# Kernel optimization log

Measured on AMD Instinct MI355X. Metric: run time of the kernel, lower is better.

Reference implementation:

```python
import jax, jax.numpy as jnp
import numpy as np

GRID_MIN, GRID_MAX, NUM_GRIDS = -2.0, 2.0, 8
DENOM = (GRID_MAX - GRID_MIN) / (NUM_GRIDS - 1)
DIM, NUM_HEADS = 768, 12
B, N = 8, 1024


def _layer_norm(x, w, b, eps=1e-5):
    mu = jnp.mean(x, axis=-1, keepdims=True)
    var = jnp.mean((x - mu) ** 2, axis=-1, keepdims=True)
    return (x - mu) * jax.lax.rsqrt(var + eps) * w + b


def _fastkan(x, ln_w, ln_b, spline_w, base_w, base_b):
    # x: [..., C]; spline_w: [C*G, O]; base_w: [C, O]
    grid = jnp.linspace(GRID_MIN, GRID_MAX, NUM_GRIDS, dtype=x.dtype)
    h = _layer_norm(x, ln_w, ln_b)
    # RBF basis expansion: [..., C, G]
    basis = jnp.exp(-(((h[..., None] - grid) / DENOM) ** 2))
    basis = basis.reshape(*basis.shape[:-2], -1)  # [..., C*G]
    ret = basis @ spline_w
    ret = ret + jax.nn.silu(x) @ base_w + base_b
    return ret


def setup_inputs() -> dict:
    key = jax.random.key(0)
    ks = jax.random.split(key, 6)
    C = DIM
    return {
        "x": jax.random.normal(ks[0], (B, N, C), jnp.float32),
        "qkv_ln_w": jnp.ones((C,), jnp.float32),
        "qkv_ln_b": jnp.zeros((C,), jnp.float32),
        "qkv_spline_w": jax.random.normal(ks[1], (C * NUM_GRIDS, 3 * C), jnp.float32) * 0.1,
        "qkv_base_w": jax.random.normal(ks[2], (C, 3 * C), jnp.float32) * (1.0 / np.sqrt(C)),
        "qkv_base_b": jnp.zeros((3 * C,), jnp.float32),
        "proj_ln_w": jnp.ones((C,), jnp.float32),
        "proj_ln_b": jnp.zeros((C,), jnp.float32),
        "proj_spline_w": jax.random.normal(ks[3], (C * NUM_GRIDS, C), jnp.float32) * 0.1,
        "proj_base_w": jax.random.normal(ks[4], (C, C), jnp.float32) * (1.0 / np.sqrt(C)),
        "proj_base_b": jnp.zeros((C,), jnp.float32),
    }


def reference(x, qkv_ln_w, qkv_ln_b, qkv_spline_w, qkv_base_w, qkv_base_b,
              proj_ln_w, proj_ln_b, proj_spline_w, proj_base_w, proj_base_b):
    b, n, c = x.shape
    h = NUM_HEADS
    d = c // h
    scale = d ** -0.5
    qkv = _fastkan(x, qkv_ln_w, qkv_ln_b, qkv_spline_w, qkv_base_w, qkv_base_b)
    qkv = qkv.reshape(b, n, 3, h, d).transpose(2, 0, 3, 1, 4)  # [3,B,H,N,D]
    q, k, v = qkv[0], qkv[1], qkv[2]
    attn = jnp.einsum("bhnd,bhmd->bhnm", q, k) * scale
    attn = jax.nn.softmax(attn, axis=-1)
    out = jnp.einsum("bhnm,bhmd->bhnd", attn, v)
    out = out.transpose(0, 2, 1, 3).reshape(b, n, c)
    out = _fastkan(out, proj_ln_w, proj_ln_b, proj_spline_w, proj_base_w, proj_base_b)
    return out
```

## Files before the change

kernel.cpp:

```cpp
#include <hip/hip_runtime.h>
#include <cstdint>
#include <cstddef>

typedef _Float16 h8 __attribute__((ext_vector_type(8)));
typedef float f4 __attribute__((ext_vector_type(4)));
typedef float f16f __attribute__((ext_vector_type(16)));

#define DEV static __device__ __forceinline__

DEV void gld16(const void* g, void* l) {
  __builtin_amdgcn_global_load_lds(
      (const __attribute__((address_space(1))) void*)g,
      (__attribute__((address_space(3))) void*)l, 16, 0, 0);
}

__global__ __launch_bounds__(256)
void kan_prep(const float* __restrict__ X, const float* __restrict__ lnw,
              const float* __restrict__ lnb, _Float16* __restrict__ Acat) {
  const int row = blockIdx.x;
  const int tid = threadIdx.x;
  const float* xr = X + (size_t)row * 768;
  float xv[3];
  xv[0] = xr[tid]; xv[1] = xr[tid + 256]; xv[2] = xr[tid + 512];
  float s = xv[0] + xv[1] + xv[2];
  float q = xv[0] * xv[0] + xv[1] * xv[1] + xv[2] * xv[2];
#pragma unroll
  for (int off = 32; off; off >>= 1) {
    s += __shfl_xor(s, off);
    q += __shfl_xor(q, off);
  }
  __shared__ float rs_[4], rq_[4];
  const int wave = tid >> 6;
  if ((tid & 63) == 0) { rs_[wave] = s; rq_[wave] = q; }
  __syncthreads();
  s = rs_[0] + rs_[1] + rs_[2] + rs_[3];
  q = rq_[0] + rq_[1] + rq_[2] + rq_[3];
  const float mu = s * (1.0f / 768.0f);
  const float var = q * (1.0f / 768.0f) - mu * mu;
  const float rsig = rsqrtf(var + 1e-5f);
  _Float16* out = Acat + (size_t)row * 6912;
#pragma unroll
  for (int i = 0; i < 3; ++i) {
    const int c = tid + i * 256;
    const float x = xv[i];
    const float h = (x - mu) * rsig * lnw[c] + lnb[c];
    union { h8 v; _Float16 u[8]; } bs;
#pragma unroll
    for (int g = 0; g < 8; ++g) {
      const float gv = -2.0f + (4.0f / 7.0f) * (float)g;
      const float t = (h - gv) * 1.75f;
      bs.u[g] = (_Float16)__expf(-t * t);
    }
    *(h8*)(out + c * 8) = bs.v;
    out[6144 + c] = (_Float16)(x / (1.0f + __expf(-x)));
  }
}

__global__ __launch_bounds__(256)
void wt_cast(const float* __restrict__ W, _Float16* __restrict__ Bp,
             int N, int koff, int nkt) {
  __shared__ float t[32][33];
  const int k0 = blockIdx.x * 32, n0 = blockIdx.y * 32;
  const int tx = threadIdx.x & 31, ty = threadIdx.x >> 5;
#pragma unroll
  for (int i = 0; i < 4; ++i)
    t[ty + i * 8][tx] = W[(size_t)(k0 + ty + i * 8) * N + n0 + tx];
  __syncthreads();
  const int f = threadIdx.x;
  if (f < 128) {
    const int nn = f & 31, cc = f >> 5;
    union { h8 v; _Float16 u[8]; } bs;
#pragma unroll
    for (int j = 0; j < 8; ++j) bs.u[j] = (_Float16)t[cc * 8 + j][nn];
    const int kg = koff + k0 + cc * 8;
    const int nt = (n0 + nn) >> 5;
    const size_t addr = ((size_t)nt * nkt + (kg >> 6)) * 2048 +
                        (size_t)((((kg >> 4) & 3) * 64 + nn + 32 * ((kg >> 3) & 1))) * 8;
    *(h8*)(Bp + addr) = bs.v;
  }
}

__global__ __launch_bounds__(256)
void v_transpose(const _Float16* __restrict__ qkv, _Float16* __restrict__ Vt) {
  const int bh = blockIdx.z, hh = bh % 12, b = bh / 12;
  const int kvb = blockIdx.x * 32, db = blockIdx.y * 32;
  __shared__ _Float16 t[32][33];
  const int tx = threadIdx.x & 31, ty = threadIdx.x >> 5;
#pragma unroll
  for (int i = 0; i < 4; ++i) {
    const int kv = kvb + ty + i * 8;
    t[ty + i * 8][tx] = qkv[(size_t)(b * 1024 + kv) * 2304 + 1536 + hh * 64 + db + tx];
  }
  __syncthreads();
#pragma unroll
  for (int i = 0; i < 4; ++i) {
    const int d = db + ty + i * 8;
    Vt[(size_t)(bh * 64 + d) * 1024 + kvb + tx] = t[tx][ty + i * 8];
  }
}

template <bool F16OUT>
__global__ __launch_bounds__(256, 3)
void gemm_bt(const _Float16* __restrict__ A, const _Float16* __restrict__ Bp,
             const float* __restrict__ bias, void* __restrict__ Cout,
             int N, int ldK, int kLen, size_t sliceStride) {
  __shared__ __align__(16) _Float16 As[128 * 64];
  const int tid = threadIdx.x;
  const int lane = tid & 63, wave = tid >> 6;
  const int bm = blockIdx.y * 128, bn = blockIdx.x * 128;
  const int slice = blockIdx.z;
  const int kOff = slice * kLen;
  const int rsub = lane >> 3;
  const int l7 = lane & 7;
  const int l31 = lane & 31, half = lane >> 5;
  const int wm = (wave >> 1) * 64, wn = (wave & 1) * 64;
  const _Float16* ap[4];
  _Float16* al[4];
#pragma unroll
  for (int i = 0; i < 4; ++i) {
    const int ch = wave * 4 + i;
    const int ksw = (l7 ^ rsub ^ ((ch & 3) << 1)) * 8;
    ap[i] = A + (size_t)(bm + ch * 8 + rsub) * ldK + kOff + ksw;
    al[i] = As + ch * 512;
  }
  const size_t nktTot = (size_t)(ldK >> 6);
  const int kt0 = kOff >> 6;
  const _Float16* bpp[2];
#pragma unroll
  for (int ni = 0; ni < 2; ++ni)
    bpp[ni] = Bp + ((size_t)((bn >> 5) + (wn >> 5) + ni) * nktTot + kt0) * 2048 + lane * 8;

  f16f acc[2][2] = {};
  const int swz = l7 ^ ((rsub & 3) << 1);
  const int nkt = kLen >> 6;
  for (int kt = 0; kt < nkt; ++kt) {
    h8 breg[2][4];
#pragma unroll
    for (int ni = 0; ni < 2; ++ni)
#pragma unroll
      for (int ks = 0; ks < 4; ++ks)
        breg[ni][ks] = *(const h8*)(bpp[ni] + ks * 512);
#pragma unroll
    for (int i = 0; i < 4; ++i) {
      gld16(ap[i], al[i]);
      ap[i] += 64;
    }
#pragma unroll
    for (int ni = 0; ni < 2; ++ni) bpp[ni] += 2048;
    __syncthreads();
    const h8* A8 = (const h8*)As;
#pragma unroll
    for (int ks = 0; ks < 4; ++ks) {
      const int o = (ks * 2 + half) ^ swz;
      h8 af[2];
#pragma unroll
      for (int mi = 0; mi < 2; ++mi) af[mi] = A8[(wm + mi * 32 + l31) * 8 + o];
#pragma unroll
      for (int mi = 0; mi < 2; ++mi)
#pragma unroll
        for (int ni = 0; ni < 2; ++ni)
          acc[mi][ni] = __builtin_amdgcn_mfma_f32_32x32x16_f16(af[mi], breg[ni][ks], acc[mi][ni], 0, 0, 0);
    }
    __syncthreads();
  }
#pragma unroll
  for (int ni = 0; ni < 2; ++ni) {
    const int col = bn + wn + ni * 32 + l31;
    const float bv = F16OUT ? bias[col] : 0.0f;
#pragma unroll
    for (int mi = 0; mi < 2; ++mi) {
      const int rb = bm + wm + mi * 32 + 4 * half;
#pragma unroll
      for (int reg = 0; reg < 16; ++reg) {
        const int r = rb + (reg & 3) + 8 * (reg >> 2);
        const float v = acc[mi][ni][reg] + bv;
        if (F16OUT)
          ((_Float16*)Cout)[(size_t)r * N + col] = (_Float16)v;
        else
          ((float*)Cout + slice * sliceStride)[(size_t)r * N + col] = v;
      }
    }
  }
}

__global__ __launch_bounds__(256)
void ksum2(const float* __restrict__ P, const float* __restrict__ bias,
           float* __restrict__ out) {
  const size_t off = ((size_t)blockIdx.x * 256 + threadIdx.x) * 4;
  const int col = (int)(off % 768);
  f4 a = *(const f4*)(P + off);
  f4 b = *(const f4*)(P + (size_t)8192 * 768 + off);
  f4 c = *(const f4*)(bias + col);
  *(f4*)(out + off) = a + b + c;
}

__global__ __launch_bounds__(256)
void attn(const _Float16* __restrict__ qkv, const _Float16* __restrict__ Vt,
          float* __restrict__ ctx) {
  __shared__ __align__(16) _Float16 Qs[128 * 64];
  __shared__ __align__(16) _Float16 Ks[64 * 64];
  __shared__ __align__(16) _Float16 Vs[64 * 64];
  __shared__ __align__(16) _Float16 Ps[4 * 32 * 72];
  const int tid = threadIdx.x;
  const int lane = tid & 63, wave = tid >> 6;
  const int bh = blockIdx.y, hh = bh % 12, b = bh / 12;
  const int qt = blockIdx.x;
  const int rsub = lane >> 3;
  const int ksw = ((lane & 7) ^ rsub) * 8;
#pragma unroll
  for (int i = 0; i < 4; ++i) {
    const int ch = wave * 4 + i;
    const int row = ch * 8 + rsub;
    gld16(qkv + (size_t)(b * 1024 + qt * 128 + row) * 2304 + hh * 64 + ksw, Qs + ch * 512);
  }
  const int l16 = lane & 15, quad = lane >> 4, r7 = l16 & 7;
  f4 acc_o[2][4] = {};
  float m_old[2][4], l_sum[2][4];
#pragma unroll
  for (int mi = 0; mi < 2; ++mi)
#pragma unroll
    for (int j = 0; j < 4; ++j) { m_old[mi][j] = -1e30f; l_sum[mi][j] = 0.0f; }

  _Float16* Pw = Ps + wave * (32 * 72);

  for (int kv0 = 0; kv0 < 1024; kv0 += 64) {
#pragma unroll
    for (int i = 0; i < 2; ++i) {
      const int ch = wave * 2 + i;
      const int row = ch * 8 + rsub;
      gld16(qkv + (size_t)(b * 1024 + kv0 + row) * 2304 + 768 + hh * 64 + ksw, Ks + ch * 512);
      gld16(Vt + (size_t)(bh * 64 + row) * 1024 + kv0 + ksw, Vs + ch * 512);
    }
    __syncthreads();
    const h8* Q8 = (const h8*)Qs;
    const h8* K8 = (const h8*)Ks;
    const h8* V8 = (const h8*)Vs;
    f4 s[2][4] = {};
#pragma unroll
    for (int ks = 0; ks < 2; ++ks) {
      const int kq = (ks * 4 + quad) ^ r7;
      h8 qf[2], kf[4];
#pragma unroll
      for (int mi = 0; mi < 2; ++mi) qf[mi] = Q8[(wave * 32 + mi * 16 + l16) * 8 + kq];
#pragma unroll
      for (int ni = 0; ni < 4; ++ni) kf[ni] = K8[(ni * 16 + l16) * 8 + kq];
#pragma unroll
      for (int mi = 0; mi < 2; ++mi)
#pragma unroll
        for (int ni = 0; ni < 4; ++ni)
          s[mi][ni] = __builtin_amdgcn_mfma_f32_16x16x32_f16(qf[mi], kf[ni], s[mi][ni], 0, 0, 0);
    }
#pragma unroll
    for (int mi = 0; mi < 2; ++mi)
#pragma unroll
      for (int ni = 0; ni < 4; ++ni) s[mi][ni] *= 0.125f;
#pragma unroll
    for (int mi = 0; mi < 2; ++mi) {
#pragma unroll
      for (int j = 0; j < 4; ++j) {
        float vm = fmaxf(fmaxf(s[mi][0][j], s[mi][1][j]), fmaxf(s[mi][2][j], s[mi][3][j]));
#pragma unroll
        for (int off = 1; off < 16; off <<= 1) vm = fmaxf(vm, __shfl_xor(vm, off));
        const float mn = fmaxf(m_old[mi][j], vm);
        const float alpha = __expf(m_old[mi][j] - mn);
        float rs = 0.0f;
#pragma unroll
        for (int ni = 0; ni < 4; ++ni) {
          const float p = __expf(s[mi][ni][j] - mn);
          s[mi][ni][j] = p;
          rs += p;
        }
#pragma unroll
        for (int off = 1; off < 16; off <<= 1) rs += __shfl_xor(rs, off);
        l_sum[mi][j] = l_sum[mi][j] * alpha + rs;
        m_old[mi][j] = mn;
#pragma unroll
        for (int ni = 0; ni < 4; ++ni) acc_o[mi][ni][j] *= alpha;
      }
    }
#pragma unroll
    for (int mi = 0; mi < 2; ++mi)
#pragma unroll
      for (int ni = 0; ni < 4; ++ni)
#pragma unroll
        for (int j = 0; j < 4; ++j)
          Pw[(mi * 16 + quad * 4 + j) * 72 + ni * 16 + l16] = (_Float16)s[mi][ni][j];
#pragma unroll
    for (int ks = 0; ks < 2; ++ks) {
      const int kq = ks * 4 + quad;
      h8 pf[2], vf[4];
#pragma unroll
      for (int mi = 0; mi < 2; ++mi) pf[mi] = *(const h8*)(Pw + (mi * 16 + l16) * 72 + kq * 8);
#pragma unroll
      for (int ni = 0; ni < 4; ++ni) vf[ni] = V8[(ni * 16 + l16) * 8 + (kq ^ r7)];
#pragma unroll
      for (int mi = 0; mi < 2; ++mi)
#pragma unroll
        for (int ni = 0; ni < 4; ++ni)
          acc_o[mi][ni] = __builtin_amdgcn_mfma_f32_16x16x32_f16(pf[mi], vf[ni], acc_o[mi][ni], 0, 0, 0);
    }
    __syncthreads();
  }
#pragma unroll
  for (int mi = 0; mi < 2; ++mi) {
#pragma unroll
    for (int j = 0; j < 4; ++j) {
      const float inv = 1.0f / l_sum[mi][j];
      const int tok = b * 1024 + qt * 128 + wave * 32 + mi * 16 + quad * 4 + j;
      float* cr = ctx + (size_t)tok * 768 + hh * 64;
#pragma unroll
      for (int ni = 0; ni < 4; ++ni) cr[ni * 16 + l16] = acc_o[mi][ni][j] * inv;
    }
  }
}

extern "C" void kernel_launch(void* const* d_in, const int* in_sizes, int n_in,
                              void* d_out, int out_size, void* d_ws, size_t ws_size,
                              hipStream_t stream) {
  (void)in_sizes; (void)n_in; (void)out_size; (void)ws_size;
  const float* x    = (const float*)d_in[0];
  const float* qlnw = (const float*)d_in[1];
  const float* qlnb = (const float*)d_in[2];
  const float* qsw  = (const float*)d_in[3];
  const float* qbw  = (const float*)d_in[4];
  const float* qbb  = (const float*)d_in[5];
  const float* plnw = (const float*)d_in[6];
  const float* plnb = (const float*)d_in[7];
  const float* psw  = (const float*)d_in[8];
  const float* pbw  = (const float*)d_in[9];
  const float* pbb  = (const float*)d_in[10];
  float* out = (float*)d_out;

  _Float16* WtQ  = (_Float16*)d_ws;
  _Float16* WtP  = WtQ + (size_t)2304 * 6912;
  _Float16* Acat = WtP + (size_t)768 * 6912;
  _Float16* QKV  = Acat + (size_t)8192 * 6912;
  _Float16* Vt   = QKV + (size_t)8192 * 2304;
  float* CTX = (float*)(Vt + (size_t)96 * 64 * 1024);
  float* Pp = (float*)QKV;

  dim3 blk(256);
  wt_cast<<<dim3(192, 72), blk, 0, stream>>>(qsw, WtQ, 2304, 0, 108);
  wt_cast<<<dim3(24, 72),  blk, 0, stream>>>(qbw, WtQ, 2304, 6144, 108);
  wt_cast<<<dim3(192, 24), blk, 0, stream>>>(psw, WtP, 768, 0, 108);
  wt_cast<<<dim3(24, 24),  blk, 0, stream>>>(pbw, WtP, 768, 6144, 108);
  kan_prep<<<8192, blk, 0, stream>>>(x, qlnw, qlnb, Acat);
  gemm_bt<true><<<dim3(2304 / 128, 8192 / 128, 1), blk, 0, stream>>>(
      Acat, WtQ, qbb, QKV, 2304, 6912, 6912, 0);
  v_transpose<<<dim3(32, 2, 96), blk, 0, stream>>>(QKV, Vt);
  attn<<<dim3(8, 96), blk, 0, stream>>>(QKV, Vt, CTX);
  kan_prep<<<8192, blk, 0, stream>>>(CTX, plnw, plnb, Acat);
  gemm_bt<false><<<dim3(768 / 128, 8192 / 128, 2), blk, 0, stream>>>(
      Acat, WtP, nullptr, Pp, 768, 6912, 3456, (size_t)8192 * 768);
  ksum2<<<8192 * 768 / 4 / 256, blk, 0, stream>>>(Pp, pbb, out);
}
```

Measured before the change: 762.6 us.

## Double-buffer A tiles and B registers in gemm_bt with XCD-aware block remap

Software-pipelines the GEMM main loop: A tiles go to alternating LDS buffers and B fragments to alternating register sets, so the next K tile is fetched while MFMAs run on the current one. This hides global load latency behind compute. It also remaps block indices so that each XCD handles a contiguous band of M rows, aiming for better L2 reuse. In exchange, LDS use doubles and launch bounds drop to 2 blocks per CU. The remap assumes gridDim.y is divisible by 8, and the loop handles an odd tile count only through its guards.

```diff
diff --git a/kernel.cpp b/kernel.cpp
--- a/kernel.cpp
+++ b/kernel.cpp
@@ -99,15 +99,51 @@
   }
 }
 
+#define LOAD_B(dst)                                       \
+  {                                                       \
+    _Pragma("unroll") for (int ni = 0; ni < 2; ++ni) {    \
+      _Pragma("unroll") for (int ks = 0; ks < 4; ++ks)    \
+        dst[ni][ks] = *(const h8*)(bpp[ni] + ks * 512);   \
+      bpp[ni] += 2048;                                    \
+    }                                                     \
+  }
+#define LOAD_A(buf)                                       \
+  {                                                       \
+    _Pragma("unroll") for (int i = 0; i < 4; ++i) {       \
+      gld16(ap[i], (buf) + alOff[i]);                     \
+      ap[i] += 64;                                        \
+    }                                                     \
+  }
+#define MFMA_STEP(buf, br)                                \
+  {                                                       \
+    const h8* A8 = (const h8*)(buf);                      \
+    _Pragma("unroll") for (int ks = 0; ks < 4; ++ks) {    \
+      const int o = (ks * 2 + half) ^ swz;                \
+      h8 af0 = A8[(wm + l31) * 8 + o];                    \
+      h8 af1 = A8[(wm + 32 + l31) * 8 + o];               \
+      acc[0][0] = __builtin_amdgcn_mfma_f32_32x32x16_f16(af0, br[0][ks], acc[0][0], 0, 0, 0); \
+      acc[0][1] = __builtin_amdgcn_mfma_f32_32x32x16_f16(af0, br[1][ks], acc[0][1], 0, 0, 0); \
+      acc[1][0] = __builtin_amdgcn_mfma_f32_32x32x16_f16(af1, br[0][ks], acc[1][0], 0, 0, 0); \
+      acc[1][1] = __builtin_amdgcn_mfma_f32_32x32x16_f16(af1, br[1][ks], acc[1][1], 0, 0, 0); \
+    }                                                     \
+  }
+
 template <bool F16OUT>
-__global__ __launch_bounds__(256, 3)
+__global__ __launch_bounds__(256, 2)
 void gemm_bt(const _Float16* __restrict__ A, const _Float16* __restrict__ Bp,
              const float* __restrict__ bias, void* __restrict__ Cout,
              int N, int ldK, int kLen, size_t sliceStride) {
-  __shared__ __align__(16) _Float16 As[128 * 64];
+  __shared__ __align__(16) _Float16 As[2 * 128 * 64];
+  _Float16* As0 = As;
+  _Float16* As1 = As + 128 * 64;
   const int tid = threadIdx.x;
   const int lane = tid & 63, wave = tid >> 6;
-  const int bm = blockIdx.y * 128, bn = blockIdx.x * 128;
+  const int gx = gridDim.x;
+  const int lin = blockIdx.y * gx + blockIdx.x;
+  const int xcd = lin & 7, pos = lin >> 3;
+  const int bandH = gridDim.y >> 3;
+  const int bm = (xcd * bandH + pos / gx) * 128;
+  const int bn = (pos % gx) * 128;
   const int slice = blockIdx.z;
   const int kOff = slice * kLen;
   const int rsub = lane >> 3;
@@ -115,13 +151,13 @@
   const int l31 = lane & 31, half = lane >> 5;
   const int wm = (wave >> 1) * 64, wn = (wave & 1) * 64;
   const _Float16* ap[4];
-  _Float16* al[4];
+  int alOff[4];
 #pragma unroll
   for (int i = 0; i < 4; ++i) {
     const int ch = wave * 4 + i;
     const int ksw = (l7 ^ rsub ^ ((ch & 3) << 1)) * 8;
     ap[i] = A + (size_t)(bm + ch * 8 + rsub) * ldK + kOff + ksw;
-    al[i] = As + ch * 512;
+    alOff[i] = ch * 512;
   }
   const size_t nktTot = (size_t)(ldK >> 6);
   const int kt0 = kOff >> 6;
@@ -133,35 +169,16 @@
   f16f acc[2][2] = {};
   const int swz = l7 ^ ((rsub & 3) << 1);
   const int nkt = kLen >> 6;
-  for (int kt = 0; kt < nkt; ++kt) {
-    h8 breg[2][4];
-#pragma unroll
-    for (int ni = 0; ni < 2; ++ni)
-#pragma unroll
-      for (int ks = 0; ks < 4; ++ks)
-        breg[ni][ks] = *(const h8*)(bpp[ni] + ks * 512);
-#pragma unroll
-    for (int i = 0; i < 4; ++i) {
-      gld16(ap[i], al[i]);
-      ap[i] += 64;
-    }
-#pragma unroll
-    for (int ni = 0; ni < 2; ++ni) bpp[ni] += 2048;
+  h8 bregA[2][4], bregB[2][4];
+  LOAD_B(bregA);
+  LOAD_A(As0);
+  for (int kt = 0; kt < nkt; kt += 2) {
     __syncthreads();
-    const h8* A8 = (const h8*)As;
-#pragma unroll
-    for (int ks = 0; ks < 4; ++ks) {
-      const int o = (ks * 2 + half) ^ swz;
-      h8 af[2];
-#pragma unroll
-      for (int mi = 0; mi < 2; ++mi) af[mi] = A8[(wm + mi * 32 + l31) * 8 + o];
-#pragma unroll
-      for (int mi = 0; mi < 2; ++mi)
-#pragma unroll
-        for (int ni = 0; ni < 2; ++ni)
-          acc[mi][ni] = __builtin_amdgcn_mfma_f32_32x32x16_f16(af[mi], breg[ni][ks], acc[mi][ni], 0, 0, 0);
-    }
+    if (kt + 1 < nkt) { LOAD_B(bregB); LOAD_A(As1); }
+    MFMA_STEP(As0, bregA);
     __syncthreads();
+    if (kt + 2 < nkt) { LOAD_B(bregA); LOAD_A(As0); }
+    MFMA_STEP(As1, bregB);
   }
 #pragma unroll
   for (int ni = 0; ni < 2; ++ni) {
```

Result: faster. 698.8 us (-8.4%).

## Fuse RBF basis expansion into GEMM A-operand generation, store only normalized h

Applied to the files above, without the earlier changes.

Stops materializing the full 8x-expanded fp16 basis matrix. The prep kernel now writes normalized h transposed per channel, plus SiLU values in an MFMA fragment layout. The GEMM recomputes the eight RBF exponentials in registers per fragment, loads B directly into double-buffered registers, and drops the LDS A tile and barriers. This cuts global traffic for the large A matrix. The cost is much more exp work inside the GEMM (every N-tile block recomputes it), scattered 2-byte Ht loads, lower occupancy (launch bounds 2), and a grid swapped so blocks iterate M fastest.

```diff
diff --git a/kernel.cpp b/kernel.cpp
--- a/kernel.cpp
+++ b/kernel.cpp
@@ -14,45 +14,63 @@
       (__attribute__((address_space(3))) void*)l, 16, 0, 0);
 }
 
-__global__ __launch_bounds__(256)
-void kan_prep(const float* __restrict__ X, const float* __restrict__ lnw,
-              const float* __restrict__ lnb, _Float16* __restrict__ Acat) {
-  const int row = blockIdx.x;
-  const int tid = threadIdx.x;
-  const float* xr = X + (size_t)row * 768;
-  float xv[3];
-  xv[0] = xr[tid]; xv[1] = xr[tid + 256]; xv[2] = xr[tid + 512];
-  float s = xv[0] + xv[1] + xv[2];
-  float q = xv[0] * xv[0] + xv[1] * xv[1] + xv[2] * xv[2];
-#pragma unroll
-  for (int off = 32; off; off >>= 1) {
-    s += __shfl_xor(s, off);
-    q += __shfl_xor(q, off);
-  }
-  __shared__ float rs_[4], rq_[4];
-  const int wave = tid >> 6;
-  if ((tid & 63) == 0) { rs_[wave] = s; rq_[wave] = q; }
+DEV h8 rbf8(float h) {
+  const float a = fmaf(h, 1.75f, 3.5f);
+  union { h8 v; _Float16 u[8]; } o;
+#pragma unroll
+  for (int g = 0; g < 8; ++g) {
+    const float d = a - (float)g;
+    o.u[g] = (_Float16)__expf(-d * d);
+  }
+  return o.v;
+}
+
+__global__ __launch_bounds__(256)
+void kan_prep2(const float* __restrict__ X, const float* __restrict__ lnw,
+               const float* __restrict__ lnb, _Float16* __restrict__ Ht,
+               _Float16* __restrict__ Sf) {
+  const int mb = blockIdx.x;
+  const int R = mb * 32;
+  const int t = threadIdx.x;
+  __shared__ float mu_[32], rs_[32];
+  {
+    const int r = t >> 3, p = t & 7;
+    const float* xr = X + (size_t)(R + r) * 768;
+    float s = 0.f, q = 0.f;
+    for (int i = 0; i < 96; ++i) {
+      const float v = xr[p + 8 * i];
+      s += v; q += v * v;
+    }
+    s += __shfl_xor(s, 1); q += __shfl_xor(q, 1);
+    s += __shfl_xor(s, 2); q += __shfl_xor(q, 2);
+    s += __shfl_xor(s, 4); q += __shfl_xor(q, 4);
+    if (p == 0) {
+      const float mu = s * (1.f / 768.f);
+      mu_[r] = mu;
+      rs_[r] = rsqrtf(q * (1.f / 768.f) - mu * mu + 1e-5f);
+    }
+  }
   __syncthreads();
-  s = rs_[0] + rs_[1] + rs_[2] + rs_[3];
-  q = rq_[0] + rq_[1] + rq_[2] + rq_[3];
-  const float mu = s * (1.0f / 768.0f);
-  const float var = q * (1.0f / 768.0f) - mu * mu;
-  const float rsig = rsqrtf(var + 1e-5f);
-  _Float16* out = Acat + (size_t)row * 6912;
-#pragma unroll
-  for (int i = 0; i < 3; ++i) {
-    const int c = tid + i * 256;
-    const float x = xv[i];
-    const float h = (x - mu) * rsig * lnw[c] + lnb[c];
-    union { h8 v; _Float16 u[8]; } bs;
+  const int r = t & 31, cb = t >> 5;
+  const float mu = mu_[r], rsg = rs_[r];
+  for (int i = 0; i < 96; ++i) {
+    const int c = cb + 8 * i;
+    const float x = X[(size_t)(R + r) * 768 + c];
+    const float h = (x - mu) * rsg * lnw[c] + lnb[c];
+    Ht[(size_t)c * 8192 + R + r] = (_Float16)h;
+  }
+  for (int j = 0; j < 12; ++j) {
+    const int cc = cb + 8 * j;
+    const float* xp = X + (size_t)(R + r) * 768 + cc * 8;
+    union { h8 v; _Float16 u[8]; } sv;
 #pragma unroll
     for (int g = 0; g < 8; ++g) {
-      const float gv = -2.0f + (4.0f / 7.0f) * (float)g;
-      const float t = (h - gv) * 1.75f;
-      bs.u[g] = (_Float16)__expf(-t * t);
-    }
-    *(h8*)(out + c * 8) = bs.v;
-    out[6144 + c] = (_Float16)(x / (1.0f + __expf(-x)));
+      const float x = xp[g];
+      sv.u[g] = (_Float16)(x / (1.f + __expf(-x)));
+    }
+    const size_t addr = ((size_t)mb * 12 + (cc >> 3)) * 2048 +
+                        (size_t)(((cc >> 1) & 3) * 64 + r + 32 * (cc & 1)) * 8;
+    *(h8*)(Sf + addr) = sv.v;
   }
 }
 
@@ -99,69 +117,77 @@
   }
 }
 
+#define LOADB(dst, ktv)                                                   \
+  { _Pragma("unroll") for (int ni = 0; ni < 2; ++ni)                      \
+      _Pragma("unroll") for (int ks = 0; ks < 4; ++ks)                    \
+        dst[ni][ks] = *(const h8*)(bpp[ni] + (size_t)(ktv) * 2048 + ks * 512); }
+
+#define LOADH(dst, kgv)                                                   \
+  { _Pragma("unroll") for (int mi = 0; mi < 2; ++mi)                      \
+      _Pragma("unroll") for (int ks = 0; ks < 4; ++ks)                    \
+        dst[mi][ks] = Ht[(size_t)((kgv) * 8 + ks * 2 + half) * 8192 + am0 + mi * 32]; }
+
+#define STEP(bc, hc, kgv)                                                 \
+  {                                                                       \
+    if ((kgv) < 96) {                                                     \
+      _Pragma("unroll") for (int ks = 0; ks < 4; ++ks) {                  \
+        h8 a0 = rbf8((float)hc[0][ks]);                                   \
+        h8 a1 = rbf8((float)hc[1][ks]);                                   \
+        acc[0][0] = __builtin_amdgcn_mfma_f32_32x32x16_f16(a0, bc[0][ks], acc[0][0], 0, 0, 0); \
+        acc[0][1] = __builtin_amdgcn_mfma_f32_32x32x16_f16(a0, bc[1][ks], acc[0][1], 0, 0, 0); \
+        acc[1][0] = __builtin_amdgcn_mfma_f32_32x32x16_f16(a1, bc[0][ks], acc[1][0], 0, 0, 0); \
+        acc[1][1] = __builtin_amdgcn_mfma_f32_32x32x16_f16(a1, bc[1][ks], acc[1][1], 0, 0, 0); \
+      }                                                                   \
+    } else {                                                              \
+      const size_t tb = (size_t)((kgv) - 96) * 2048;                      \
+      _Pragma("unroll") for (int ks = 0; ks < 4; ++ks) {                  \
+        h8 a0 = *(const h8*)(Sf + sfB0 + tb + ks * 512);                  \
+        h8 a1 = *(const h8*)(Sf + sfB1 + tb + ks * 512);                  \
+        acc[0][0] = __builtin_amdgcn_mfma_f32_32x32x16_f16(a0, bc[0][ks], acc[0][0], 0, 0, 0); \
+        acc[0][1] = __builtin_amdgcn_mfma_f32_32x32x16_f16(a0, bc[1][ks], acc[0][1], 0, 0, 0); \
+        acc[1][0] = __builtin_amdgcn_mfma_f32_32x32x16_f16(a1, bc[0][ks], acc[1][0], 0, 0, 0); \
+        acc[1][1] = __builtin_amdgcn_mfma_f32_32x32x16_f16(a1, bc[1][ks], acc[1][1], 0, 0, 0); \
+      }                                                                   \
+    }                                                                     \
+  }
+
 template <bool F16OUT>
-__global__ __launch_bounds__(256, 3)
-void gemm_bt(const _Float16* __restrict__ A, const _Float16* __restrict__ Bp,
-             const float* __restrict__ bias, void* __restrict__ Cout,
-             int N, int ldK, int kLen, size_t sliceStride) {
-  __shared__ __align__(16) _Float16 As[128 * 64];
+__global__ __launch_bounds__(256, 2)
+void gemm_fused(const _Float16* __restrict__ Ht, const _Float16* __restrict__ Sf,
+                const _Float16* __restrict__ Bp, const float* __restrict__ bias,
+                void* __restrict__ Cout, int N, int ktPerSlice, int nktTot,
+                size_t sliceStride) {
   const int tid = threadIdx.x;
   const int lane = tid & 63, wave = tid >> 6;
-  const int bm = blockIdx.y * 128, bn = blockIdx.x * 128;
+  const int bm = blockIdx.x * 128, bn = blockIdx.y * 128;
   const int slice = blockIdx.z;
-  const int kOff = slice * kLen;
-  const int rsub = lane >> 3;
-  const int l7 = lane & 7;
+  const int kt0 = slice * ktPerSlice;
   const int l31 = lane & 31, half = lane >> 5;
   const int wm = (wave >> 1) * 64, wn = (wave & 1) * 64;
-  const _Float16* ap[4];
-  _Float16* al[4];
-#pragma unroll
-  for (int i = 0; i < 4; ++i) {
-    const int ch = wave * 4 + i;
-    const int ksw = (l7 ^ rsub ^ ((ch & 3) << 1)) * 8;
-    ap[i] = A + (size_t)(bm + ch * 8 + rsub) * ldK + kOff + ksw;
-    al[i] = As + ch * 512;
-  }
-  const size_t nktTot = (size_t)(ldK >> 6);
-  const int kt0 = kOff >> 6;
+  const int am0 = bm + wm + l31;
+  const size_t sfB0 = ((size_t)((bm + wm) >> 5) * 12) * 2048 + (size_t)(l31 + 32 * half) * 8;
+  const size_t sfB1 = ((size_t)((bm + wm + 32) >> 5) * 12) * 2048 + (size_t)(l31 + 32 * half) * 8;
   const _Float16* bpp[2];
 #pragma unroll
   for (int ni = 0; ni < 2; ++ni)
-    bpp[ni] = Bp + ((size_t)((bn >> 5) + (wn >> 5) + ni) * nktTot + kt0) * 2048 + lane * 8;
+    bpp[ni] = Bp + ((size_t)(((bn + wn) >> 5) + ni) * nktTot + kt0) * 2048 + lane * 8;
 
   f16f acc[2][2] = {};
-  const int swz = l7 ^ ((rsub & 3) << 1);
-  const int nkt = kLen >> 6;
-  for (int kt = 0; kt < nkt; ++kt) {
-    h8 breg[2][4];
-#pragma unroll
-    for (int ni = 0; ni < 2; ++ni)
-#pragma unroll
-      for (int ks = 0; ks < 4; ++ks)
-        breg[ni][ks] = *(const h8*)(bpp[ni] + ks * 512);
-#pragma unroll
-    for (int i = 0; i < 4; ++i) {
-      gld16(ap[i], al[i]);
-      ap[i] += 64;
-    }
-#pragma unroll
-    for (int ni = 0; ni < 2; ++ni) bpp[ni] += 2048;
-    __syncthreads();
-    const h8* A8 = (const h8*)As;
-#pragma unroll
-    for (int ks = 0; ks < 4; ++ks) {
-      const int o = (ks * 2 + half) ^ swz;
-      h8 af[2];
-#pragma unroll
-      for (int mi = 0; mi < 2; ++mi) af[mi] = A8[(wm + mi * 32 + l31) * 8 + o];
-#pragma unroll
-      for (int mi = 0; mi < 2; ++mi)
-#pragma unroll
-        for (int ni = 0; ni < 2; ++ni)
-          acc[mi][ni] = __builtin_amdgcn_mfma_f32_32x32x16_f16(af[mi], breg[ni][ks], acc[mi][ni], 0, 0, 0);
-    }
-    __syncthreads();
+  h8 bA[2][4], bB[2][4];
+  _Float16 hA[2][4], hB[2][4];
+  LOADB(bA, 0);
+  if (kt0 < 96) LOADH(hA, kt0);
+  const int nkt = ktPerSlice;
+  for (int kt = 0; kt < nkt; kt += 2) {
+    const int kg0 = kt0 + kt, kg1 = kg0 + 1;
+    LOADB(bB, kt + 1);
+    if (kg1 < 96) LOADH(hB, kg1);
+    STEP(bA, hA, kg0);
+    if (kt + 2 < nkt) {
+      LOADB(bA, kt + 2);
+      if (kg0 + 2 < 96) LOADH(hA, kg0 + 2);
+    }
+    STEP(bB, hB, kg1);
   }
 #pragma unroll
   for (int ni = 0; ni < 2; ++ni) {
@@ -331,11 +357,12 @@
   const float* pbb  = (const float*)d_in[10];
   float* out = (float*)d_out;
 
-  _Float16* WtQ  = (_Float16*)d_ws;
-  _Float16* WtP  = WtQ + (size_t)2304 * 6912;
-  _Float16* Acat = WtP + (size_t)768 * 6912;
-  _Float16* QKV  = Acat + (size_t)8192 * 6912;
-  _Float16* Vt   = QKV + (size_t)8192 * 2304;
+  _Float16* WtQ = (_Float16*)d_ws;
+  _Float16* WtP = WtQ + (size_t)2304 * 6912;
+  _Float16* Ht  = WtP + (size_t)768 * 6912;
+  _Float16* Sf  = Ht + (size_t)768 * 8192;
+  _Float16* QKV = Sf + (size_t)256 * 12 * 2048;
+  _Float16* Vt  = QKV + (size_t)8192 * 2304;
   float* CTX = (float*)(Vt + (size_t)96 * 64 * 1024);
   float* Pp = (float*)QKV;
 
@@ -344,13 +371,13 @@
   wt_cast<<<dim3(24, 72),  blk, 0, stream>>>(qbw, WtQ, 2304, 6144, 108);
   wt_cast<<<dim3(192, 24), blk, 0, stream>>>(psw, WtP, 768, 0, 108);
   wt_cast<<<dim3(24, 24),  blk, 0, stream>>>(pbw, WtP, 768, 6144, 108);
-  kan_prep<<<8192, blk, 0, stream>>>(x, qlnw, qlnb, Acat);
-  gemm_bt<true><<<dim3(2304 / 128, 8192 / 128, 1), blk, 0, stream>>>(
-      Acat, WtQ, qbb, QKV, 2304, 6912, 6912, 0);
+  kan_prep2<<<256, blk, 0, stream>>>(x, qlnw, qlnb, Ht, Sf);
+  gemm_fused<true><<<dim3(64, 18, 1), blk, 0, stream>>>(
+      Ht, Sf, WtQ, qbb, QKV, 2304, 108, 108, 0);
   v_transpose<<<dim3(32, 2, 96), blk, 0, stream>>>(QKV, Vt);
   attn<<<dim3(8, 96), blk, 0, stream>>>(QKV, Vt, CTX);
-  kan_prep<<<8192, blk, 0, stream>>>(CTX, plnw, plnb, Acat);
-  gemm_bt<false><<<dim3(768 / 128, 8192 / 128, 2), blk, 0, stream>>>(
-      Acat, WtP, nullptr, Pp, 768, 6912, 3456, (size_t)8192 * 768);
+  kan_prep2<<<256, blk, 0, stream>>>(CTX, plnw, plnb, Ht, Sf);
+  gemm_fused<false><<<dim3(64, 6, 2), blk, 0, stream>>>(
+      Ht, Sf, WtP, nullptr, Pp, 768, 54, 108, (size_t)8192 * 768);
   ksum2<<<8192 * 768 / 4 / 256, blk, 0, stream>>>(Pp, pbb, out);
 }
```

Result: slower. 918.2 us (+20.4%).
